# Kernel optimization log

Hardware: AMD Instinct MI355X
Metric: run time of the kernel (lower is better)

Reference implementation:

```python
import jax, jax.numpy as jnp
import numpy as np

N = 100000      # nodes
E = 3200000     # edges
IN_DIM = 128
HID = 128
OUT_DIM = 1
LAYERS = 8
ALPHA = 0.1
THETA = 0.5


def setup_inputs() -> dict:
    key = jax.random.key(0)
    ks = jax.random.split(key, 8)
    x = jax.random.normal(ks[0], (N, IN_DIM), dtype=jnp.float32)
    edge_index = jax.random.randint(ks[1], (2, E), 0, N, dtype=jnp.int64)
    edge_weight = jax.random.uniform(ks[2], (E,), dtype=jnp.float32)  # unused by original forward path
    W_in = jax.random.normal(ks[3], (IN_DIM, HID), dtype=jnp.float32) * 0.05
    b_in = jnp.zeros((HID,), dtype=jnp.float32)
    W_gcn = jax.random.normal(ks[4], (LAYERS, HID, HID), dtype=jnp.float32) * 0.05
    W_out = jax.random.normal(ks[5], (HID, OUT_DIM), dtype=jnp.float32) * 0.05
    b_out = jnp.zeros((OUT_DIM,), dtype=jnp.float32)
    return {"x": x, "edge_weight": edge_weight, "W_in": W_in, "b_in": b_in,
            "W_gcn": W_gcn, "W_out": W_out, "b_out": b_out, "edge_index": edge_index}


def _gcn_norm(edge_index, dtype):
    # add self loops (fill value 1), symmetric normalization deg^-1/2 A deg^-1/2
    sl = jnp.arange(N, dtype=edge_index.dtype)
    row = jnp.concatenate([edge_index[0], sl])
    col = jnp.concatenate([edge_index[1], sl])
    w = jnp.ones(row.shape[0], dtype=dtype)
    deg = jax.ops.segment_sum(w, col, num_segments=N)
    dinv = jnp.where(deg > 0, jax.lax.rsqrt(deg), 0.0)
    norm = dinv[row] * dinv[col]
    return row, col, norm


def reference(x, edge_weight, W_in, b_in, W_gcn, W_out, b_out, edge_index):
    row, col, norm = _gcn_norm(edge_index, x.dtype)
    h = x @ W_in + b_in            # initial_proj
    h0 = h                          # residual x0
    for i in range(LAYERS):
        # dropout is identity in eval mode
        msg = h[row] * norm[:, None]                       # gather + scale [E+N, HID]
        agg = jax.ops.segment_sum(msg, col, num_segments=N)
        s = (1.0 - ALPHA) * agg + ALPHA * h0               # identity-mapped residual
        beta = float(np.log(THETA / (i + 1) + 1.0))
        h = (1.0 - beta) * s + beta * (s @ W_gcn[i])       # GCNII weight mix
        h = jax.nn.relu(h)
    return h @ W_out + b_out
```

## Files before the change

kernel.cpp:

```cpp
#include <hip/hip_runtime.h>
#include <hip/hip_bf16.h>
#include <math.h>

#define N_NODES 100000
#define N_EDGES 3200000
#define HID 128
#define LAYERS 8
#define ALPHA 0.1f
#define THETA 0.5f

#define NBKT 391
#define BKT_STRIDE 10240
#define EPT 16
#define CHUNK 4096

typedef unsigned int uint;
typedef unsigned short ushort;
typedef __attribute__((ext_vector_type(8))) short short8;
typedef __attribute__((ext_vector_type(4))) float f32x4;

__device__ inline float bf_lo(uint p) { return __uint_as_float(p << 16); }
__device__ inline float bf_hi(uint p) { return __uint_as_float(p & 0xffff0000u); }
__device__ inline uint bf_pack(float x, float y) {
    uint ux = __float_as_uint(x), uy = __float_as_uint(y);
    uint rx = (ux + 0x7fffu + ((ux >> 16) & 1u)) >> 16;
    uint ry = (uy + 0x7fffu + ((uy >> 16) & 1u)) >> 16;
    return rx | (ry << 16);
}
__device__ inline ushort bfr(float x) {
    uint u = __float_as_uint(x);
    return (ushort)((u + 0x7fffu + ((u >> 16) & 1u)) >> 16);
}
__device__ inline float bff(ushort s) { return __uint_as_float(((uint)s) << 16); }

__global__ __launch_bounds__(256) void k_bucket(const int* __restrict__ rowi,
                                                const int* __restrict__ coli,
                                                uint* __restrict__ eb,
                                                int* __restrict__ gcnt) {
    __shared__ int bcnt[NBKT];
    __shared__ int gbase[NBKT];
    int t = threadIdx.x;
    for (int i = t; i < NBKT; i += 256) bcnt[i] = 0;
    __syncthreads();

    int e0 = blockIdx.x * CHUNK;
    int bk[EPT];
    int rk[EPT];
    uint rec[EPT];
#pragma unroll
    for (int j = 0; j < EPT; ++j) {
        int e = e0 + j * 256 + t;
        if (e < N_EDGES) {
            int r = rowi[e];
            int c = coli[e];
            bk[j] = c >> 8;
            rec[j] = ((uint)r << 8) | (uint)(c & 255);
            rk[j] = atomicAdd(&bcnt[bk[j]], 1);
        } else {
            bk[j] = -1;
        }
    }
    __syncthreads();
    for (int i = t; i < NBKT; i += 256) {
        int n = bcnt[i];
        gbase[i] = n ? atomicAdd(&gcnt[i], n) : 0;
    }
    __syncthreads();
#pragma unroll
    for (int j = 0; j < EPT; ++j) {
        if (bk[j] >= 0)
            eb[(size_t)bk[j] * BKT_STRIDE + gbase[bk[j]] + rk[j]] = rec[j];
    }
}

__global__ __launch_bounds__(512) void k_bscan(const int* __restrict__ gcnt,
                                               int* __restrict__ bbase) {
    __shared__ int lds[512];
    int t = threadIdx.x;
    int v = (t < NBKT) ? gcnt[t] : 0;
    lds[t] = v;
    __syncthreads();
    for (int off = 1; off < 512; off <<= 1) {
        int u = (t >= off) ? lds[t - off] : 0;
        __syncthreads();
        lds[t] += u;
        __syncthreads();
    }
    if (t < NBKT) bbase[t] = lds[t] - v;
}

__global__ __launch_bounds__(256) void k_node_ipt(const uint* __restrict__ eb,
                                                  const int* __restrict__ gcnt,
                                                  const int* __restrict__ bbase,
                                                  float* __restrict__ dinv,
                                                  int* __restrict__ indptr) {
    __shared__ int ncnt[256];
    __shared__ int sc[256];
    int b = blockIdx.x;
    int t = threadIdx.x;
    ncnt[t] = 0;
    __syncthreads();
    int ne = gcnt[b];
    const uint* ebp = eb + (size_t)b * BKT_STRIDE;
    for (int i = t; i < ne; i += 256) atomicAdd(&ncnt[ebp[i] & 255], 1);
    __syncthreads();
    int v = ncnt[t];
    sc[t] = v;
    __syncthreads();
    for (int off = 1; off < 256; off <<= 1) {
        int u = (t >= off) ? sc[t - off] : 0;
        __syncthreads();
        sc[t] += u;
        __syncthreads();
    }
    int node = b * 256 + t;
    if (node < N_NODES) {
        dinv[node] = rsqrtf((float)(v + 1));
        indptr[node] = bbase[b] + (sc[t] - v);
    }
    if (b == NBKT - 1 && t == 255) indptr[N_NODES] = N_EDGES;
}

__global__ __launch_bounds__(256) void k_fill2(const uint* __restrict__ eb,
                                               const int* __restrict__ gcnt,
                                               const int* __restrict__ indptr,
                                               int* __restrict__ csr) {
    __shared__ int scur[256];
    __shared__ int sipt[256];
    int b = blockIdx.x;
    int t = threadIdx.x;
    int node = b * 256 + t;
    sipt[t] = (node < N_NODES) ? indptr[node] : 0;
    scur[t] = 0;
    __syncthreads();
    int ne = gcnt[b];
    const uint* ebp = eb + (size_t)b * BKT_STRIDE;
    for (int i = t; i < ne; i += 256) {
        uint rec = ebp[i];
        int lc = rec & 255;
        int pos = sipt[lc] + atomicAdd(&scur[lc], 1);
        csr[pos] = (int)(rec >> 8);
    }
}

__global__ __launch_bounds__(256) void k_wprep(const float* __restrict__ Wg,
                                               ushort* __restrict__ Wt) {
    int l = blockIdx.x;
    const float* W = Wg + (size_t)l * HID * HID;
    ushort* T = Wt + (size_t)l * HID * HID;
    int t = threadIdx.x;
#pragma unroll
    for (int i = 0; i < 16; ++i) {
        int idx = t + 256 * i;
        int k = idx >> 5;
        int c4 = idx & 31;
        float4 v = *(const float4*)(W + (size_t)k * HID + c4 * 4);
        T[(c4 * 4 + 0) * HID + k] = bfr(v.x);
        T[(c4 * 4 + 1) * HID + k] = bfr(v.y);
        T[(c4 * 4 + 2) * HID + k] = bfr(v.z);
        T[(c4 * 4 + 3) * HID + k] = bfr(v.w);
    }
}

__global__ __launch_bounds__(256) void k_spmm(const uint* __restrict__ h,
                                              const uint* __restrict__ h0,
                                              const float* __restrict__ dinv,
                                              const int* __restrict__ indptr,
                                              const int* __restrict__ csr,
                                              uint* __restrict__ s_out) {
    int node = blockIdx.x * 8 + (threadIdx.x >> 5);
    if (node >= N_NODES) return;
    int l = threadIdx.x & 31;
    int beg = indptr[node];
    int end = indptr[node + 1];
    float di = dinv[node];
    uint2 hs = *(const uint2*)(h + node * 64 + l * 2);
    uint2 h0v = *(const uint2*)(h0 + node * 64 + l * 2);
    float a0[2] = {0.f, 0.f}, a1[2] = {0.f, 0.f};
    float a2[2] = {0.f, 0.f}, a3[2] = {0.f, 0.f};
    int e = beg;
    for (; e + 8 <= end; e += 8) {
        int sr[8];
#pragma unroll
        for (int j = 0; j < 8; ++j) sr[j] = csr[e + j];
        float dv[8];
#pragma unroll
        for (int j = 0; j < 8; ++j) dv[j] = dinv[sr[j]];
        uint2 p[8];
#pragma unroll
        for (int j = 0; j < 8; ++j) p[j] = *(const uint2*)(h + sr[j] * 64 + l * 2);
#pragma unroll
        for (int j = 0; j < 8; ++j) {
            float w = dv[j];
            int d = j & 1;
            a0[d] = fmaf(w, bf_lo(p[j].x), a0[d]);
            a1[d] = fmaf(w, bf_hi(p[j].x), a1[d]);
            a2[d] = fmaf(w, bf_lo(p[j].y), a2[d]);
            a3[d] = fmaf(w, bf_hi(p[j].y), a3[d]);
        }
    }
    for (; e < end; e += 2) {
        int sr[2];
        float w[2];
#pragma unroll
        for (int j = 0; j < 2; ++j) {
            int idx = e + j;
            sr[j] = csr[idx < end ? idx : beg];
            w[j] = (idx < end) ? dinv[sr[j]] : 0.f;
        }
        uint2 p[2];
#pragma unroll
        for (int j = 0; j < 2; ++j) p[j] = *(const uint2*)(h + sr[j] * 64 + l * 2);
#pragma unroll
        for (int j = 0; j < 2; ++j) {
            a0[j] = fmaf(w[j], bf_lo(p[j].x), a0[j]);
            a1[j] = fmaf(w[j], bf_hi(p[j].x), a1[j]);
            a2[j] = fmaf(w[j], bf_lo(p[j].y), a2[j]);
            a3[j] = fmaf(w[j], bf_hi(p[j].y), a3[j]);
        }
    }
    float s0 = a0[0] + a0[1];
    float s1 = a1[0] + a1[1];
    float s2 = a2[0] + a2[1];
    float s3 = a3[0] + a3[1];
    float sc = (1.0f - ALPHA) * di;
    float rx = sc * fmaf(di, bf_lo(hs.x), s0) + ALPHA * bf_lo(h0v.x);
    float ry = sc * fmaf(di, bf_hi(hs.x), s1) + ALPHA * bf_hi(h0v.x);
    float rz = sc * fmaf(di, bf_lo(hs.y), s2) + ALPHA * bf_lo(h0v.y);
    float rw = sc * fmaf(di, bf_hi(hs.y), s3) + ALPHA * bf_hi(h0v.y);
    uint2 o;
    o.x = bf_pack(rx, ry);
    o.y = bf_pack(rz, rw);
    *(uint2*)(s_out + node * 64 + l * 2) = o;
}

__global__ __launch_bounds__(256) void k_gemm_in(const float* __restrict__ A,
                                                 const float* __restrict__ W,
                                                 const float* __restrict__ bias,
                                                 uint* __restrict__ out0) {
    __shared__ float sT[32 * 64];
    __shared__ float Ws[32 * 128];
    int t = threadIdx.x;
    int tr = t & 15;
    int tc = t >> 4;
    int rowBase = blockIdx.x * 64;
    float acc[4][8] = {};

    for (int ko = 0; ko < HID; ko += 32) {
#pragma unroll
        for (int pass = 0; pass < 2; ++pass) {
            int lin = t + 256 * pass;
            int r = lin >> 3;
            int kq = lin & 7;
            int ar = rowBase + r;
            if (ar >= N_NODES) ar = N_NODES - 1;
            float4 v = *(const float4*)(A + (size_t)ar * HID + ko + 4 * kq);
            sT[(4 * kq + 0) * 64 + r] = v.x;
            sT[(4 * kq + 1) * 64 + r] = v.y;
            sT[(4 * kq + 2) * 64 + r] = v.z;
            sT[(4 * kq + 3) * 64 + r] = v.w;
        }
#pragma unroll
        for (int pass = 0; pass < 4; ++pass) {
            int lin = t + 256 * pass;
            int k = lin >> 5;
            int c4 = lin & 31;
            *(float4*)&Ws[k * 128 + 4 * c4] =
                *(const float4*)(W + (size_t)(ko + k) * HID + 4 * c4);
        }
        __syncthreads();
#pragma unroll
        for (int k = 0; k < 32; ++k) {
            float4 a = *(const float4*)&sT[k * 64 + 4 * tr];
            float4 w0 = *(const float4*)&Ws[k * 128 + 8 * tc];
            float4 w1 = *(const float4*)&Ws[k * 128 + 8 * tc + 4];
            float av[4] = {a.x, a.y, a.z, a.w};
            float wv[8] = {w0.x, w0.y, w0.z, w0.w, w1.x, w1.y, w1.z, w1.w};
#pragma unroll
            for (int i = 0; i < 4; ++i)
#pragma unroll
                for (int j = 0; j < 8; ++j)
                    acc[i][j] = fmaf(av[i], wv[j], acc[i][j]);
        }
        __syncthreads();
    }

    int c0 = 8 * tc;
    float bb[8];
#pragma unroll
    for (int j = 0; j < 8; ++j) bb[j] = bias[c0 + j];
#pragma unroll
    for (int i = 0; i < 4; ++i) {
        int r = rowBase + 4 * tr + i;
        if (r >= N_NODES) break;
        float v[8];
#pragma unroll
        for (int j = 0; j < 8; ++j) v[j] = acc[i][j] + bb[j];
        uint4 o;
        o.x = bf_pack(v[0], v[1]);
        o.y = bf_pack(v[2], v[3]);
        o.z = bf_pack(v[4], v[5]);
        o.w = bf_pack(v[6], v[7]);
        *(uint4*)(out0 + (size_t)r * 64 + c0 / 2) = o;
    }
}

#define SAS 136

__global__ __launch_bounds__(256) void k_gemm_layer(const uint* __restrict__ A,
                                                    const ushort* __restrict__ Wt,
                                                    uint* __restrict__ out0,
                                                    float beta,
                                                    const float* __restrict__ Wo,
                                                    const float* __restrict__ b_out,
                                                    float* __restrict__ outf) {
    __shared__ ushort sA[64 * SAS];
    __shared__ ushort pack[64 * 128];
    __shared__ float sWo[128];
    int t = threadIdx.x;
    int lane = t & 63;
    int wv = t >> 6;
    int rowBase = blockIdx.x * 64;

#pragma unroll
    for (int i = 0; i < 4; ++i) {
        int idx = t + 256 * i;
        int r = idx >> 4;
        int q = idx & 15;
        int ar = rowBase + r;
        if (ar >= N_NODES) ar = N_NODES - 1;
        uint4 v = *(const uint4*)(A + (size_t)ar * 64 + q * 4);
        *(uint4*)((uint*)(sA + r * SAS) + q * 4) = v;
    }
    if (Wo != nullptr && t < 128) sWo[t] = Wo[t];
    __syncthreads();

    int fr = lane & 15;
    int fq = lane >> 4;
    const ushort* Wb0 = Wt + (size_t)(wv * 32 + fr) * HID;
    const ushort* Wb1 = Wt + (size_t)(wv * 32 + 16 + fr) * HID;
    f32x4 acc[4][2] = {};
#pragma unroll
    for (int kc = 0; kc < 4; ++kc) {
        int kof = kc * 32 + fq * 8;
        short8 b0 = *(const short8*)(Wb0 + kof);
        short8 b1 = *(const short8*)(Wb1 + kof);
#pragma unroll
        for (int tm = 0; tm < 4; ++tm) {
            short8 a = *(const short8*)(sA + (tm * 16 + fr) * SAS + kof);
            acc[tm][0] = __builtin_amdgcn_mfma_f32_16x16x32_bf16(a, b0, acc[tm][0], 0, 0, 0);
            acc[tm][1] = __builtin_amdgcn_mfma_f32_16x16x32_bf16(a, b1, acc[tm][1], 0, 0, 0);
        }
    }

    float ob = 1.0f - beta;
#pragma unroll
    for (int tm = 0; tm < 4; ++tm)
#pragma unroll
        for (int tn = 0; tn < 2; ++tn)
#pragma unroll
            for (int r = 0; r < 4; ++r) {
                int row = tm * 16 + fq * 4 + r;
                int col = wv * 32 + tn * 16 + fr;
                float sv = bff(sA[row * SAS + col]);
                float val = fmaxf(fmaf(ob, sv, beta * acc[tm][tn][r]), 0.f);
                pack[row * 128 + col] = bfr(val);
            }
    __syncthreads();

    if (Wo == nullptr) {
#pragma unroll
        for (int i = 0; i < 4; ++i) {
            int idx = t + 256 * i;
            int r = idx >> 4;
            int q = idx & 15;
            int ar = rowBase + r;
            if (ar < N_NODES)
                *(uint4*)(out0 + (size_t)ar * 64 + q * 4) =
                    *(const uint4*)((const uint*)(pack + r * 128) + q * 4);
        }
    } else {
        int row = t >> 2;
        int sub = t & 3;
        const ushort* pr_row = pack + row * 128 + sub * 32;
        float pr = 0.f;
#pragma unroll
        for (int i = 0; i < 32; i += 2) {
            uint pp = *(const uint*)(pr_row + i);
            pr = fmaf(bf_lo(pp), sWo[sub * 32 + i], pr);
            pr = fmaf(bf_hi(pp), sWo[sub * 32 + i + 1], pr);
        }
        pr += __shfl_xor(pr, 1);
        pr += __shfl_xor(pr, 2);
        int ar = rowBase + row;
        if (sub == 0 && ar < N_NODES) outf[ar] = pr + b_out[0];
    }
}

extern "C" void kernel_launch(void* const* d_in, const int* in_sizes, int n_in,
                              void* d_out, int out_size, void* d_ws, size_t ws_size,
                              hipStream_t stream) {
    const float* x     = (const float*)d_in[0];
    const float* W_in  = (const float*)d_in[2];
    const float* b_in  = (const float*)d_in[3];
    const float* W_gcn = (const float*)d_in[4];
    const float* W_out = (const float*)d_in[5];
    const float* b_out = (const float*)d_in[6];
    const int*   ei    = (const int*)d_in[7];
    const int* rowi = ei;
    const int* coli = ei + N_EDGES;
    float* out = (float*)d_out;

    char* ws = (char*)d_ws;
    auto alloc = [&](size_t bytes) -> char* {
        char* p = ws;
        ws += (bytes + 255) & ~(size_t)255;
        return p;
    };
    float*  dinv    = (float*) alloc((size_t)N_NODES * 4);
    int*    indptr  = (int*)   alloc((size_t)(N_NODES + 1) * 4);
    int*    gcnt    = (int*)   alloc(2048 * 4);
    int*    bbase   = (int*)   alloc(2048 * 4);
    int*    csr     = (int*)   alloc((size_t)N_EDGES * 4);
    ushort* Wt      = (ushort*)alloc((size_t)LAYERS * HID * HID * 2);
    uint*   hA      = (uint*)  alloc((size_t)N_NODES * 64 * 4);
    uint*   hB      = (uint*)  alloc((size_t)N_NODES * 64 * 4);
    uint*   h0      = (uint*)  alloc((size_t)N_NODES * 64 * 4);
    uint*   eb      = hB;

    hipMemsetAsync(gcnt, 0, (size_t)NBKT * 4, stream);

    k_bucket<<<(N_EDGES + CHUNK - 1) / CHUNK, 256, 0, stream>>>(rowi, coli, eb, gcnt);
    k_bscan<<<1, 512, 0, stream>>>(gcnt, bbase);
    k_node_ipt<<<NBKT, 256, 0, stream>>>(eb, gcnt, bbase, dinv, indptr);
    k_fill2<<<NBKT, 256, 0, stream>>>(eb, gcnt, indptr, csr);
    k_wprep<<<LAYERS, 256, 0, stream>>>(W_gcn, Wt);

    int gemm_blocks = (N_NODES + 63) / 64;
    k_gemm_in<<<gemm_blocks, 256, 0, stream>>>(x, W_in, b_in, h0);

    for (int l = 0; l < LAYERS; ++l) {
        const uint* hsrc = (l == 0) ? h0 : hA;
        k_spmm<<<(N_NODES + 7) / 8, 256, 0, stream>>>(hsrc, h0, dinv, indptr,
                                                      csr, hB);
        float beta = logf(THETA / (float)(l + 1) + 1.0f);
        bool last = (l == LAYERS - 1);
        k_gemm_layer<<<gemm_blocks, 256, 0, stream>>>(
            hB, Wt + (size_t)l * HID * HID, hA, beta,
            last ? W_out : nullptr, b_out, out);
    }
}
```

Before: 1.298 ms.

## Split SpMM into two feature-half passes to shrink gather working set

The aggregation kernel now processes half of the feature columns per launch, with each lane loading one packed bf16 pair instead of two, and is launched twice per layer with a column offset. The intent is to halve the gathered feature working set per pass so random neighbor row reads hit cache more often. The unroll is widened to 16 edges with four accumulators to keep enough loads in flight. In exchange, the CSR indices and dinv values are read twice per layer and per-lane loads become narrower.

```diff
diff --git a/kernel.cpp b/kernel.cpp
--- a/kernel.cpp
+++ b/kernel.cpp
@@ -162,76 +162,65 @@
     }
 }
 
-__global__ __launch_bounds__(256) void k_spmm(const uint* __restrict__ h,
-                                              const uint* __restrict__ h0,
-                                              const float* __restrict__ dinv,
-                                              const int* __restrict__ indptr,
-                                              const int* __restrict__ csr,
-                                              uint* __restrict__ s_out) {
+__global__ __launch_bounds__(256) void k_spmm_h(const uint* __restrict__ h,
+                                                const uint* __restrict__ h0,
+                                                const float* __restrict__ dinv,
+                                                const int* __restrict__ indptr,
+                                                const int* __restrict__ csr,
+                                                uint* __restrict__ s_out,
+                                                int fofs) {
     int node = blockIdx.x * 8 + (threadIdx.x >> 5);
     if (node >= N_NODES) return;
-    int l = threadIdx.x & 31;
+    int col = fofs + (threadIdx.x & 31);
     int beg = indptr[node];
     int end = indptr[node + 1];
     float di = dinv[node];
-    uint2 hs = *(const uint2*)(h + node * 64 + l * 2);
-    uint2 h0v = *(const uint2*)(h0 + node * 64 + l * 2);
-    float a0[2] = {0.f, 0.f}, a1[2] = {0.f, 0.f};
-    float a2[2] = {0.f, 0.f}, a3[2] = {0.f, 0.f};
+    uint hs = h[node * 64 + col];
+    uint h0v = h0[node * 64 + col];
+    float ax[4] = {0.f, 0.f, 0.f, 0.f};
+    float ay[4] = {0.f, 0.f, 0.f, 0.f};
     int e = beg;
-    for (; e + 8 <= end; e += 8) {
-        int sr[8];
-#pragma unroll
-        for (int j = 0; j < 8; ++j) sr[j] = csr[e + j];
-        float dv[8];
-#pragma unroll
-        for (int j = 0; j < 8; ++j) dv[j] = dinv[sr[j]];
-        uint2 p[8];
-#pragma unroll
-        for (int j = 0; j < 8; ++j) p[j] = *(const uint2*)(h + sr[j] * 64 + l * 2);
-#pragma unroll
-        for (int j = 0; j < 8; ++j) {
-            float w = dv[j];
-            int d = j & 1;
-            a0[d] = fmaf(w, bf_lo(p[j].x), a0[d]);
-            a1[d] = fmaf(w, bf_hi(p[j].x), a1[d]);
-            a2[d] = fmaf(w, bf_lo(p[j].y), a2[d]);
-            a3[d] = fmaf(w, bf_hi(p[j].y), a3[d]);
-        }
-    }
-    for (; e < end; e += 2) {
-        int sr[2];
-        float w[2];
-#pragma unroll
-        for (int j = 0; j < 2; ++j) {
+    for (; e + 16 <= end; e += 16) {
+        int sr[16];
+#pragma unroll
+        for (int j = 0; j < 16; ++j) sr[j] = csr[e + j];
+        float dv[16];
+#pragma unroll
+        for (int j = 0; j < 16; ++j) dv[j] = dinv[sr[j]];
+        uint p[16];
+#pragma unroll
+        for (int j = 0; j < 16; ++j) p[j] = h[sr[j] * 64 + col];
+#pragma unroll
+        for (int j = 0; j < 16; ++j) {
+            int d = j & 3;
+            ax[d] = fmaf(dv[j], bf_lo(p[j]), ax[d]);
+            ay[d] = fmaf(dv[j], bf_hi(p[j]), ay[d]);
+        }
+    }
+    for (; e < end; e += 4) {
+        int sr[4];
+        float w[4];
+#pragma unroll
+        for (int j = 0; j < 4; ++j) {
             int idx = e + j;
             sr[j] = csr[idx < end ? idx : beg];
             w[j] = (idx < end) ? dinv[sr[j]] : 0.f;
         }
-        uint2 p[2];
-#pragma unroll
-        for (int j = 0; j < 2; ++j) p[j] = *(const uint2*)(h + sr[j] * 64 + l * 2);
-#pragma unroll
-        for (int j = 0; j < 2; ++j) {
-            a0[j] = fmaf(w[j], bf_lo(p[j].x), a0[j]);
-            a1[j] = fmaf(w[j], bf_hi(p[j].x), a1[j]);
-            a2[j] = fmaf(w[j], bf_lo(p[j].y), a2[j]);
-            a3[j] = fmaf(w[j], bf_hi(p[j].y), a3[j]);
-        }
-    }
-    float s0 = a0[0] + a0[1];
-    float s1 = a1[0] + a1[1];
-    float s2 = a2[0] + a2[1];
-    float s3 = a3[0] + a3[1];
+        uint p[4];
+#pragma unroll
+        for (int j = 0; j < 4; ++j) p[j] = h[sr[j] * 64 + col];
+#pragma unroll
+        for (int j = 0; j < 4; ++j) {
+            ax[j] = fmaf(w[j], bf_lo(p[j]), ax[j]);
+            ay[j] = fmaf(w[j], bf_hi(p[j]), ay[j]);
+        }
+    }
+    float s0 = (ax[0] + ax[1]) + (ax[2] + ax[3]);
+    float s1 = (ay[0] + ay[1]) + (ay[2] + ay[3]);
     float sc = (1.0f - ALPHA) * di;
-    float rx = sc * fmaf(di, bf_lo(hs.x), s0) + ALPHA * bf_lo(h0v.x);
-    float ry = sc * fmaf(di, bf_hi(hs.x), s1) + ALPHA * bf_hi(h0v.x);
-    float rz = sc * fmaf(di, bf_lo(hs.y), s2) + ALPHA * bf_lo(h0v.y);
-    float rw = sc * fmaf(di, bf_hi(hs.y), s3) + ALPHA * bf_hi(h0v.y);
-    uint2 o;
-    o.x = bf_pack(rx, ry);
-    o.y = bf_pack(rz, rw);
-    *(uint2*)(s_out + node * 64 + l * 2) = o;
+    float rx = sc * fmaf(di, bf_lo(hs), s0) + ALPHA * bf_lo(h0v);
+    float ry = sc * fmaf(di, bf_hi(hs), s1) + ALPHA * bf_hi(h0v);
+    s_out[node * 64 + col] = bf_pack(rx, ry);
 }
 
 __global__ __launch_bounds__(256) void k_gemm_in(const float* __restrict__ A,
@@ -437,12 +426,15 @@
     k_wprep<<<LAYERS, 256, 0, stream>>>(W_gcn, Wt);
 
     int gemm_blocks = (N_NODES + 63) / 64;
+    int spmm_blocks = (N_NODES + 7) / 8;
     k_gemm_in<<<gemm_blocks, 256, 0, stream>>>(x, W_in, b_in, h0);
 
     for (int l = 0; l < LAYERS; ++l) {
         const uint* hsrc = (l == 0) ? h0 : hA;
-        k_spmm<<<(N_NODES + 7) / 8, 256, 0, stream>>>(hsrc, h0, dinv, indptr,
-                                                      csr, hB);
+        k_spmm_h<<<spmm_blocks, 256, 0, stream>>>(hsrc, h0, dinv, indptr,
+                                                  csr, hB, 0);
+        k_spmm_h<<<spmm_blocks, 256, 0, stream>>>(hsrc, h0, dinv, indptr,
+                                                  csr, hB, 32);
         float beta = logf(THETA / (float)(l + 1) + 1.0f);
         bool last = (l == LAYERS - 1);
         k_gemm_layer<<<gemm_blocks, 256, 0, stream>>>(
```

Result: slower. 1.872 ms (+44.2%).

## Split node features into 8 column slabs so SpMM gathers stay cache-resident

Applied to the files above, without the earlier changes.

Node feature buffers are now stored as 8 slabs of 16 bf16 columns each (N x 32 bytes per slab) instead of row-major 256-byte rows. The SpMM grid is split so consecutive blocks handle the same node group across the 8 slabs, with 8 lanes per node each gathering one uint. The aim is to shrink the random-gather working set per slab (3.2 MB) so it fits in L2/LLC. The edge list and dinv are now read 8 times, and each gather is only 32 bytes. Nontemporal loads and stores are added for the streamed CSR indices, h0 and the output, and the GEMM kernels are updated to read and write the slab layout.

```diff
diff --git a/kernel.cpp b/kernel.cpp
--- a/kernel.cpp
+++ b/kernel.cpp
@@ -8,6 +8,8 @@
 #define LAYERS 8
 #define ALPHA 0.1f
 #define THETA 0.5f
+
+#define SLAB ((size_t)N_NODES * 8)
 
 #define NBKT 391
 #define BKT_STRIDE 10240
@@ -168,70 +170,49 @@
                                               const int* __restrict__ indptr,
                                               const int* __restrict__ csr,
                                               uint* __restrict__ s_out) {
-    int node = blockIdx.x * 8 + (threadIdx.x >> 5);
+    int g = blockIdx.x & 7;
+    int nb = blockIdx.x >> 3;
+    int grp = threadIdx.x >> 3;
+    int u = threadIdx.x & 7;
+    int node = nb * 32 + grp;
     if (node >= N_NODES) return;
-    int l = threadIdx.x & 31;
+    const uint* hs = h + (size_t)g * SLAB;
     int beg = indptr[node];
     int end = indptr[node + 1];
     float di = dinv[node];
-    uint2 hs = *(const uint2*)(h + node * 64 + l * 2);
-    uint2 h0v = *(const uint2*)(h0 + node * 64 + l * 2);
-    float a0[2] = {0.f, 0.f}, a1[2] = {0.f, 0.f};
-    float a2[2] = {0.f, 0.f}, a3[2] = {0.f, 0.f};
+    uint hv = hs[node * 8 + u];
+    uint h0v = __builtin_nontemporal_load(h0 + (size_t)g * SLAB + node * 8 + u);
+    float ax = 0.f, ay = 0.f, bx = 0.f, by = 0.f;
     int e = beg;
     for (; e + 8 <= end; e += 8) {
         int sr[8];
 #pragma unroll
-        for (int j = 0; j < 8; ++j) sr[j] = csr[e + j];
+        for (int j = 0; j < 8; ++j) sr[j] = __builtin_nontemporal_load(csr + e + j);
         float dv[8];
 #pragma unroll
         for (int j = 0; j < 8; ++j) dv[j] = dinv[sr[j]];
-        uint2 p[8];
-#pragma unroll
-        for (int j = 0; j < 8; ++j) p[j] = *(const uint2*)(h + sr[j] * 64 + l * 2);
+        uint p[8];
+#pragma unroll
+        for (int j = 0; j < 8; ++j) p[j] = hs[sr[j] * 8 + u];
 #pragma unroll
         for (int j = 0; j < 8; ++j) {
-            float w = dv[j];
-            int d = j & 1;
-            a0[d] = fmaf(w, bf_lo(p[j].x), a0[d]);
-            a1[d] = fmaf(w, bf_hi(p[j].x), a1[d]);
-            a2[d] = fmaf(w, bf_lo(p[j].y), a2[d]);
-            a3[d] = fmaf(w, bf_hi(p[j].y), a3[d]);
-        }
-    }
-    for (; e < end; e += 2) {
-        int sr[2];
-        float w[2];
-#pragma unroll
-        for (int j = 0; j < 2; ++j) {
-            int idx = e + j;
-            sr[j] = csr[idx < end ? idx : beg];
-            w[j] = (idx < end) ? dinv[sr[j]] : 0.f;
-        }
-        uint2 p[2];
-#pragma unroll
-        for (int j = 0; j < 2; ++j) p[j] = *(const uint2*)(h + sr[j] * 64 + l * 2);
-#pragma unroll
-        for (int j = 0; j < 2; ++j) {
-            a0[j] = fmaf(w[j], bf_lo(p[j].x), a0[j]);
-            a1[j] = fmaf(w[j], bf_hi(p[j].x), a1[j]);
-            a2[j] = fmaf(w[j], bf_lo(p[j].y), a2[j]);
-            a3[j] = fmaf(w[j], bf_hi(p[j].y), a3[j]);
-        }
-    }
-    float s0 = a0[0] + a0[1];
-    float s1 = a1[0] + a1[1];
-    float s2 = a2[0] + a2[1];
-    float s3 = a3[0] + a3[1];
+            if (j & 1) { bx = fmaf(dv[j], bf_lo(p[j]), bx); by = fmaf(dv[j], bf_hi(p[j]), by); }
+            else       { ax = fmaf(dv[j], bf_lo(p[j]), ax); ay = fmaf(dv[j], bf_hi(p[j]), ay); }
+        }
+    }
+    for (; e < end; ++e) {
+        int sr = __builtin_nontemporal_load(csr + e);
+        float dv = dinv[sr];
+        uint p = hs[sr * 8 + u];
+        ax = fmaf(dv, bf_lo(p), ax);
+        ay = fmaf(dv, bf_hi(p), ay);
+    }
+    float s0 = ax + bx, s1 = ay + by;
     float sc = (1.0f - ALPHA) * di;
-    float rx = sc * fmaf(di, bf_lo(hs.x), s0) + ALPHA * bf_lo(h0v.x);
-    float ry = sc * fmaf(di, bf_hi(hs.x), s1) + ALPHA * bf_hi(h0v.x);
-    float rz = sc * fmaf(di, bf_lo(hs.y), s2) + ALPHA * bf_lo(h0v.y);
-    float rw = sc * fmaf(di, bf_hi(hs.y), s3) + ALPHA * bf_hi(h0v.y);
-    uint2 o;
-    o.x = bf_pack(rx, ry);
-    o.y = bf_pack(rz, rw);
-    *(uint2*)(s_out + node * 64 + l * 2) = o;
+    float rx = sc * fmaf(di, bf_lo(hv), s0) + ALPHA * bf_lo(h0v);
+    float ry = sc * fmaf(di, bf_hi(hv), s1) + ALPHA * bf_hi(h0v);
+    __builtin_nontemporal_store(bf_pack(rx, ry),
+                                s_out + (size_t)g * SLAB + node * 8 + u);
 }
 
 __global__ __launch_bounds__(256) void k_gemm_in(const float* __restrict__ A,
@@ -301,7 +282,7 @@
         o.y = bf_pack(v[2], v[3]);
         o.z = bf_pack(v[4], v[5]);
         o.w = bf_pack(v[6], v[7]);
-        *(uint4*)(out0 + (size_t)r * 64 + c0 / 2) = o;
+        *(uint4*)(out0 + (size_t)(tc >> 1) * SLAB + (size_t)r * 8 + (tc & 1) * 4) = o;
     }
 }
 
@@ -329,7 +310,7 @@
         int q = idx & 15;
         int ar = rowBase + r;
         if (ar >= N_NODES) ar = N_NODES - 1;
-        uint4 v = *(const uint4*)(A + (size_t)ar * 64 + q * 4);
+        uint4 v = *(const uint4*)(A + (size_t)(q >> 1) * SLAB + (size_t)ar * 8 + (q & 1) * 4);
         *(uint4*)((uint*)(sA + r * SAS) + q * 4) = v;
     }
     if (Wo != nullptr && t < 128) sWo[t] = Wo[t];
@@ -376,7 +357,7 @@
             int q = idx & 15;
             int ar = rowBase + r;
             if (ar < N_NODES)
-                *(uint4*)(out0 + (size_t)ar * 64 + q * 4) =
+                *(uint4*)(out0 + (size_t)(q >> 1) * SLAB + (size_t)ar * 8 + (q & 1) * 4) =
                     *(const uint4*)((const uint*)(pack + r * 128) + q * 4);
         }
     } else {
@@ -437,12 +418,13 @@
     k_wprep<<<LAYERS, 256, 0, stream>>>(W_gcn, Wt);
 
     int gemm_blocks = (N_NODES + 63) / 64;
+    int spmm_blocks = 8 * ((N_NODES + 31) / 32);
     k_gemm_in<<<gemm_blocks, 256, 0, stream>>>(x, W_in, b_in, h0);
 
     for (int l = 0; l < LAYERS; ++l) {
         const uint* hsrc = (l == 0) ? h0 : hA;
-        k_spmm<<<(N_NODES + 7) / 8, 256, 0, stream>>>(hsrc, h0, dinv, indptr,
-                                                      csr, hB);
+        k_spmm<<<spmm_blocks, 256, 0, stream>>>(hsrc, h0, dinv, indptr,
+                                                csr, hB);
         float beta = logf(THETA / (float)(l + 1) + 1.0f);
         bool last = (l == LAYERS - 1);
         k_gemm_layer<<<gemm_blocks, 256, 0, stream>>>(
```

Measured after the change: 3.498 ms. 170% more time.
